# Optimization experiments

Measured on AMD Instinct MI355X. Metric: run time of the kernel, lower is better.

Reference implementation:

```python
import jax, jax.numpy as jnp
import numpy as np

N_NODE = 4095
D_EMB = 32
D_MODEL = 64
NHEADS = 8
ALPHA = 1.0
B = N_NODE + 1  # batch must equal n_node+1 (see einsum 'nm,tmd->tnd')
T = 32


def setup_inputs() -> dict:
    key = jax.random.key(0)
    ks = jax.random.split(key, 16)
    f32 = jnp.float32
    inp = {
        "q": jax.random.normal(ks[0], (B, T, D_MODEL), f32),
        "k": jax.random.normal(ks[1], (B, T, D_MODEL), f32),
        "v": jax.random.normal(ks[2], (B, T, D_MODEL), f32),
        # learned parameters (torch init is randn; scaled for numeric stability)
        "emb": jax.random.normal(ks[3], (N_NODE + 1, D_EMB), f32) * 0.05,
        "We": jax.random.normal(ks[4], (D_EMB, D_MODEL, D_MODEL), f32) * 0.05,
        "be": jax.random.normal(ks[5], (D_EMB, D_MODEL), f32) * 0.05,
        "Wq": jax.random.normal(ks[6], (D_MODEL, D_MODEL), f32) * 0.05,
        "bq": jax.random.normal(ks[7], (D_MODEL,), f32) * 0.05,
        "Wk": jax.random.normal(ks[8], (D_MODEL, D_MODEL), f32) * 0.05,
        "bk": jax.random.normal(ks[9], (D_MODEL,), f32) * 0.05,
        "Wv": jax.random.normal(ks[10], (D_MODEL, D_MODEL), f32) * 0.05,
        "bv": jax.random.normal(ks[11], (D_MODEL,), f32) * 0.05,
        "Wo": jax.random.normal(ks[12], (D_MODEL, D_MODEL), f32) * 0.05,
        "bo": jax.random.normal(ks[13], (D_MODEL,), f32) * 0.05,
    }
    return inp


def _elu(x, alpha):
    return jnp.where(x > 0, x, alpha * (jnp.exp(x) - 1.0))


def _split_heads(x, h):
    # torch.cat(torch.split(x, D//h, dim=-1), dim=0): [B,T,D] -> [h*B,T,D/h]
    b, t, d = x.shape
    return jnp.moveaxis(x.reshape(b, t, h, d // h), 2, 0).reshape(h * b, t, d // h)


def _merge_heads(x, b, h):
    # torch.cat(torch.split(x, B, dim=0), dim=-1): [h*B,T,D/h] -> [B,T,D]
    hb, t, dh = x.shape
    return jnp.moveaxis(x.reshape(h, b, t, dh), 0, 2).reshape(b, t, h * dh)


def reference(q, k, v, emb, We, be, Wq, bq, Wk, bk, Wv, bv, Wo, bo):
    Bq, Tq, D = q.shape
    h = NHEADS
    scale = (D // h) ** 0.5

    # linear projections (torch Linear: x @ W.T + b)
    q = q @ Wq.T + bq
    k = k @ Wk.T + bk
    v = v @ Wv.T + bv

    # adjacency: sum over d_emb of pairwise diff == s_i - s_j (same math, no [N,N,E] tensor)
    s = jnp.sum(emb, axis=-1)  # [N+1]
    sim = s[:, None] - s[None, :]  # [N+1, N+1]
    A = jax.nn.softmax(_elu(sim, ALPHA), axis=-1) + jnp.eye(Bq, dtype=q.dtype)

    # updateQ: adjacency-weighted diffusion + per-node weight matrices
    qt = jnp.transpose(q, (1, 0, 2))  # [T, N, D]
    W = jnp.einsum('ne,eio->nio', emb, We)  # [N, D, D]
    b = emb @ be  # [N, D]
    q_ = jnp.einsum('nm,tmd->tnd', A, qt)  # diffusion
    q_ = jnp.einsum('tnd,ndo->tno', q_, W) + b  # per-node matmul
    q = jnp.transpose(q_, (1, 0, 2))  # [N, T, D]

    # manual multi-head attention via split/cat
    qh = _split_heads(q, h)
    kh = _split_heads(k, h)
    vh = _split_heads(v, h)
    attn = jax.nn.softmax(jnp.einsum('btd,bsd->bts', qh, kh) / scale, axis=-1)
    out = jnp.einsum('bts,bsd->btd', attn, vh)
    out = _merge_heads(out, Bq, h)
    return out @ Wo.T + bo
```

## Files before the change

### kernel.cpp

```cpp
#include <hip/hip_runtime.h>
#include <hip/hip_bf16.h>

constexpr int NN  = 4096;
constexpr int DE  = 32;
constexpr int TD  = 2048;

typedef __attribute__((ext_vector_type(8))) short short8;
typedef __attribute__((ext_vector_type(4))) float f32x4;

#define MFMA16(a, b, c) __builtin_amdgcn_mfma_f32_16x16x32_bf16(a, b, c, 0, 0, 0)

__device__ inline ushort f2b(float x) {
    __hip_bfloat16 h = __float2bfloat16(x);
    union { __hip_bfloat16 h; ushort u; } c; c.h = h;
    return c.u;
}

__device__ inline float b2f(ushort u) {
    union { unsigned u; float f; } c; c.u = ((unsigned)u) << 16;
    return c.f;
}

__device__ inline short8 pack8(float4 a, float4 b) {
    short8 v;
    v[0] = (short)f2b(a.x); v[1] = (short)f2b(a.y); v[2] = (short)f2b(a.z); v[3] = (short)f2b(a.w);
    v[4] = (short)f2b(b.x); v[5] = (short)f2b(b.y); v[6] = (short)f2b(b.z); v[7] = (short)f2b(b.w);
    return v;
}

__device__ inline short8 pack8v(f32x4 a, f32x4 b) {
    short8 v;
    v[0] = (short)f2b(a[0]); v[1] = (short)f2b(a[1]); v[2] = (short)f2b(a[2]); v[3] = (short)f2b(a[3]);
    v[4] = (short)f2b(b[0]); v[5] = (short)f2b(b[1]); v[6] = (short)f2b(b[2]); v[7] = (short)f2b(b[3]);
    return v;
}

__device__ __forceinline__ short8 as_s8(f32x4 v) {
    union { f32x4 f; short8 s; } u; u.f = v; return u.s;
}

template<int OFF>
__device__ __forceinline__ f32x4 gl16(unsigned long long addr) {
    f32x4 d;
    asm volatile("global_load_dwordx4 %0, %1, off offset:%c2"
                 : "=v"(d) : "v"(addr), "n"(OFF) : "memory");
    return d;
}

template<int OFF>
__device__ __forceinline__ float gl4(unsigned long long addr) {
    float d;
    asm volatile("global_load_dword %0, %1, off offset:%c2"
                 : "=v"(d) : "v"(addr), "n"(OFF) : "memory");
    return d;
}

#define WAITV(N) asm volatile("s_waitcnt vmcnt(" #N ")" ::: "memory"); \
                 __builtin_amdgcn_sched_barrier(0)

__global__ __launch_bounds__(256) void k_prep(const float* __restrict__ emb,
                                              const float* __restrict__ We,
                                              const float* __restrict__ be,
                                              const float* __restrict__ Wk,
                                              const float* __restrict__ Wv,
                                              const float* __restrict__ Wo,
                                              float* __restrict__ s_g,
                                              ushort* __restrict__ embbf,
                                              ushort* __restrict__ WeTT,
                                              ushort* __restrict__ Wkbf,
                                              ushort* __restrict__ Wvbf,
                                              ushort* __restrict__ Wobf,
                                              float* __restrict__ bn) {
    int id = blockIdx.x, tid = threadIdx.x;
    if (id < 16) {
        int n = id * 256 + tid;
        const float4* e4 = (const float4*)(emb + n * DE);
        float s = 0.f;
#pragma unroll
        for (int i = 0; i < DE / 4; ++i) { float4 v = e4[i]; s += v.x + v.y + v.z + v.w; }
        s_g[n] = s;
    } else if (id < 144) {
        int g4 = (id - 16) * 256 + tid;
        float4 v = *(const float4*)&emb[(size_t)g4 * 4];
        ushort4 o; o.x = f2b(v.x); o.y = f2b(v.y); o.z = f2b(v.z); o.w = f2b(v.w);
        *(ushort4*)&embbf[(size_t)g4 * 4] = o;
    } else if (id < 176) {
        int e = id - 144;
#pragma unroll
        for (int u = 0; u < 4; ++u) {
            int idx0 = tid * 16 + u * 4;
            float4 v = *(const float4*)&We[(size_t)e * 4096 + idx0];
            float vv[4] = {v.x, v.y, v.z, v.w};
#pragma unroll
            for (int i = 0; i < 4; ++i) {
                int idx = idx0 + i;
                int o = idx & 63, d = idx >> 6;
                WeTT[(size_t)(o * 64 + d) * 32 + e] = f2b(vv[i]);
            }
        }
    } else if (id < 224) {
        int id5 = id - 176;
        int which = id5 >> 4, gid = (id5 & 15) * 256 + tid;
        const float* src = which == 0 ? Wk : (which == 1 ? Wv : Wo);
        ushort* dst = which == 0 ? Wkbf : (which == 1 ? Wvbf : Wobf);
        dst[gid] = f2b(src[gid]);
    } else {
        int gid = (id - 224) * 256 + tid;
        int n = gid >> 6, o = gid & 63;
        float acc = 0.f;
#pragma unroll
        for (int e = 0; e < DE; ++e) acc += emb[n * DE + e] * be[e * 64 + o];
        bn[gid] = acc;
    }
}

__global__ __launch_bounds__(256) void k_pr(const float* __restrict__ X,
                                            const float* __restrict__ W,
                                            const float* __restrict__ bias,
                                            ushort* __restrict__ Y,
                                            const float* __restrict__ s_g,
                                            int* __restrict__ perm) {
    __shared__ float ss[NN];
    int id = blockIdx.x, tid = threadIdx.x;
    if (id < 512) {
        int lane = tid & 63, wid = tid >> 6;
        int r0 = id * 256 + wid * 64;
        int l15 = lane & 15, kb = lane >> 4;
        f32x4 acc[4][4] = {};
#pragma unroll
        for (int kk = 0; kk < 2; ++kk) {
            short8 af[4], bf[4];
#pragma unroll
            for (int f = 0; f < 4; ++f) {
                const float* ap = X + (size_t)(r0 + f * 16 + l15) * 64 + kk * 32 + kb * 8;
                af[f] = pack8(*(const float4*)ap, *(const float4*)(ap + 4));
                const float* bp = W + (size_t)(f * 16 + l15) * 64 + kk * 32 + kb * 8;
                bf[f] = pack8(*(const float4*)bp, *(const float4*)(bp + 4));
            }
#pragma unroll
            for (int i = 0; i < 4; ++i)
#pragma unroll
                for (int j = 0; j < 4; ++j)
                    acc[i][j] = MFMA16(af[i], bf[j], acc[i][j]);
        }
        float bcol[4];
#pragma unroll
        for (int j = 0; j < 4; ++j) bcol[j] = bias[j * 16 + l15];
#pragma unroll
        for (int i = 0; i < 4; ++i)
#pragma unroll
            for (int j = 0; j < 4; ++j)
#pragma unroll
                for (int r = 0; r < 4; ++r)
                    Y[(size_t)(r0 + i * 16 + kb * 4 + r) * 64 + j * 16 + l15] =
                        f2b(acc[i][j][r] + bcol[j]);
    } else {
        for (int i = tid; i < NN; i += 256) ss[i] = s_g[i];
        __syncthreads();
        int g = tid >> 5, l = tid & 31;
        int n = (id - 512) * 8 + g;
        float sn = ss[n];
        int cnt = 0;
        for (int j2 = 0; j2 < 128; ++j2) {
            int m = j2 * 32 + l;
            float sm = ss[m];
            cnt += (sm < sn) || (sm == sn && m < n);
        }
        for (int off = 16; off; off >>= 1) cnt += __shfl_down(cnt, off, 32);
        if (l == 0) perm[cnt] = n;
    }
}

__global__ __launch_bounds__(256) void k_csum(const ushort* __restrict__ qp,
                                              const float* __restrict__ s_g,
                                              const int* __restrict__ perm,
                                              float* __restrict__ Cj,
                                              float* __restrict__ Cb) {
    __shared__ int ns[64];
    __shared__ float bs[64];
    int bx = blockIdx.x, by = blockIdx.y, tid = threadIdx.x;
    if (tid < 64) {
        int n = perm[bx * 64 + tid];
        ns[tid] = n;
        bs[tid] = __expf(-s_g[n]);
    }
    __syncthreads();
    int j = by * 256 + tid;
    float run[8] = {};
    for (int ii = 0; ii < 64; ++ii) {
        float qv = b2f(qp[(size_t)ns[ii] * 2048 + j]);
        float b = bs[ii], t = qv;
#pragma unroll
        for (int k2 = 0; k2 < 8; ++k2) { run[k2] += t; t *= b; }
    }
    float* cp = Cj + ((size_t)bx * 2048 + j) * 8;
    *(float4*)cp       = make_float4(run[0], run[1], run[2], run[3]);
    *(float4*)(cp + 4) = make_float4(run[4], run[5], run[6], run[7]);
    if (by == 0 && tid < 64) {
        float b = bs[tid], bk = 1.f;
#pragma unroll
        for (int k2 = 0; k2 < 8; ++k2) {
            float v = bk;
            for (int off = 32; off; off >>= 1) v += __shfl_down(v, off, 64);
            if (tid == 0) Cb[bx * 8 + k2] = v;
            bk *= b;
        }
    }
}

__global__ __launch_bounds__(256) void k_pre(const float* __restrict__ Cj,
                                             float* __restrict__ PRE,
                                             const float* __restrict__ Cb,
                                             float* __restrict__ CbPre) {
    __shared__ float sCb[512];
    int tid = threadIdx.x;
    if (blockIdx.x < 64) {
        int gid = blockIdx.x * 256 + tid;
        float run = 0.f;
#pragma unroll 8
        for (int c = 0; c < 64; ++c) {
            PRE[(size_t)c * 16384 + gid] = run;
            run += Cj[(size_t)c * 16384 + gid];
        }
        PRE[(size_t)64 * 16384 + gid] = run;
    } else {
        sCb[tid] = Cb[tid];
        sCb[tid + 256] = Cb[tid + 256];
        __syncthreads();
        if (tid < 8) {
            float run = 0.f;
            for (int c = 0; c < 64; ++c) {
                CbPre[c * 8 + tid] = run;
                run += sCb[c * 8 + tid];
            }
            CbPre[512 + tid] = run;
        }
    }
}

__global__ __launch_bounds__(256) void k_combw(const ushort* __restrict__ qp,
                                               const float* __restrict__ s_g,
                                               const int* __restrict__ perm,
                                               const float* __restrict__ PRE,
                                               const float* __restrict__ CbPre,
                                               ushort* __restrict__ qdifb,
                                               const ushort* __restrict__ embbf,
                                               const ushort* __restrict__ WeTT,
                                               ushort* __restrict__ WnT) {
    __shared__ int ns[64];
    __shared__ float sa[64], sb[64];
    int id = blockIdx.x, tid = threadIdx.x;
    if (id < 512) {
        int bx = id & 63, by = id >> 6;
        if (tid < 64) {
            int n = perm[bx * 64 + tid];
            ns[tid] = n;
            float s = s_g[n];
            sa[tid] = __expf(s);
            sb[tid] = __expf(-s);
        }
        __syncthreads();
        int j = by * 256 + tid;
        float T[8], pre[8];
        {
            const float* pp = PRE + (size_t)bx * 16384 + (size_t)j * 8;
            float4 u0 = *(const float4*)pp, u1 = *(const float4*)(pp + 4);
            pre[0] = u0.x; pre[1] = u0.y; pre[2] = u0.z; pre[3] = u0.w;
            pre[4] = u1.x; pre[5] = u1.y; pre[6] = u1.z; pre[7] = u1.w;
            const float* tp = PRE + (size_t)64 * 16384 + (size_t)j * 8;
            float4 t0 = *(const float4*)tp, t1 = *(const float4*)(tp + 4);
            T[0] = t0.x; T[1] = t0.y; T[2] = t0.z; T[3] = t0.w;
            T[4] = t1.x; T[5] = t1.y; T[6] = t1.z; T[7] = t1.w;
        }
        float TB[8], preb[8];
        {
            float4 v0 = *(const float4*)&CbPre[bx * 8], v1 = *(const float4*)&CbPre[bx * 8 + 4];
            preb[0] = v0.x; preb[1] = v0.y; preb[2] = v0.z; preb[3] = v0.w;
            preb[4] = v1.x; preb[5] = v1.y; preb[6] = v1.z; preb[7] = v1.w;
            float4 t0 = *(const float4*)&CbPre[512], t1 = *(const float4*)&CbPre[516];
            TB[0] = t0.x; TB[1] = t0.y; TB[2] = t0.z; TB[3] = t0.w;
            TB[4] = t1.x; TB[5] = t1.y; TB[6] = t1.z; TB[7] = t1.w;
        }
#pragma unroll 2
        for (int ii = 0; ii < 64; ++ii) {
            int n = ns[ii];
            float a = sa[ii], b = sb[ii];
            float g0 = 0.36787944117144233f;
            float g1 = g0 * a;
            float g2 = g1 * a * 0.5f;
            float g3 = g2 * a * (1.f / 3.f);
            float g4 = g3 * a * 0.25f;
            float g5 = g4 * a * 0.2f;
            float g6 = g5 * a * (1.f / 6.f);
            float g7 = g6 * a * (1.f / 7.f);
            float Z = a * preb[1]
                    + g0 * (TB[0] - preb[0]) + g1 * (TB[1] - preb[1])
                    + g2 * (TB[2] - preb[2]) + g3 * (TB[3] - preb[3])
                    + g4 * (TB[4] - preb[4]) + g5 * (TB[5] - preb[5])
                    + g6 * (TB[6] - preb[6]) + g7 * (TB[7] - preb[7]);
            float izv = 1.f / Z;
            float qv = b2f(qp[(size_t)n * 2048 + j]);
            float ss2 = g0 * (T[0] - pre[0]) + g1 * (T[1] - pre[1])
                      + g2 * (T[2] - pre[2]) + g3 * (T[3] - pre[3])
                      + g4 * (T[4] - pre[4]) + g5 * (T[5] - pre[5])
                      + g6 * (T[6] - pre[6]) + g7 * (T[7] - pre[7]);
            float outv = (a * pre[1] + ss2) * izv + qv;
            qdifb[(size_t)n * 2048 + j] = f2b(outv);
            float bk = 1.f;
#pragma unroll
            for (int k2 = 0; k2 < 8; ++k2) { pre[k2] += bk * qv; preb[k2] += bk; bk *= b; }
        }
    } else {
        int w2 = id - 512;
        int lane = tid & 63, wid = tid >> 6;
        int n0  = (w2 & 31) * 128 + (wid >> 1) * 64;
        int od0 = (w2 >> 5) * 128 + (wid & 1) * 64;
        int l15 = lane & 15, kb = lane >> 4;
        short8 af[4], bf[4];
#pragma unroll
        for (int f = 0; f < 4; ++f) {
            af[f] = *(const short8*)(embbf + (size_t)(n0 + f * 16 + l15) * 32 + kb * 8);
            bf[f] = *(const short8*)(WeTT + (size_t)(od0 + f * 16 + l15) * 32 + kb * 8);
        }
        f32x4 acc[4][4] = {};
#pragma unroll
        for (int i = 0; i < 4; ++i)
#pragma unroll
            for (int j = 0; j < 4; ++j)
                acc[i][j] = MFMA16(af[i], bf[j], acc[i][j]);
#pragma unroll
        for (int i = 0; i < 4; ++i)
#pragma unroll
            for (int j = 0; j < 4; ++j)
#pragma unroll
                for (int r = 0; r < 4; ++r)
                    WnT[(size_t)(n0 + i * 16 + kb * 4 + r) * 4096 + od0 + j * 16 + l15] =
                        f2b(acc[i][j][r]);
    }
}

__global__ __launch_bounds__(128, 2) void k_fused(const float* __restrict__ kin,
                                                  const float* __restrict__ vin,
                                                  const ushort* __restrict__ qdifb,
                                                  const ushort* __restrict__ WnT,
                                                  const float* __restrict__ bn,
                                                  const ushort* __restrict__ Wkbf,
                                                  const float* __restrict__ bk,
                                                  const ushort* __restrict__ Wvbf,
                                                  const float* __restrict__ bv,
                                                  const ushort* __restrict__ Wobf,
                                                  const float* __restrict__ bo,
                                                  float* __restrict__ out) {
    __shared__ ushort Kb[2][2176];
    __shared__ ushort Qb[2][2176];
    __shared__ ushort Vb[2][2560];
    __shared__ ushort Pb[2][1280];
    __shared__ ushort attb[2][2304];
    int tid = threadIdx.x, lane = tid & 63, w = tid >> 6;
    int b = blockIdx.x * 2 + w;
    int l15 = lane & 15, g = lane >> 4;
    int hh_w = l15 >> 3, d1_w = l15 & 7;
    const float SCALE = 0.35355339059327373f;
    short8 zfrag = {};

    unsigned long long bkA = (unsigned long long)(bk + 32 + l15);
    unsigned long long bnA = (unsigned long long)(bn + (size_t)b * 64 + 32 + l15);
    unsigned long long bvA = (unsigned long long)(bv + 32 + l15);
    unsigned long long boA = (unsigned long long)(bo + 32 + l15);
    unsigned long long wkA = (unsigned long long)((const char*)Wkbf + l15 * 128 + g * 16 + 3072);
    unsigned long long kaA = (unsigned long long)(kin + (size_t)b * TD + (8 + l15) * 64 + g * 8);
    unsigned long long wvA = (unsigned long long)((const char*)Wvbf + l15 * 128 + g * 16 + 3072);
    unsigned long long vaA = (unsigned long long)(vin + (size_t)b * TD + (8 + l15) * 64 + g * 8);
    unsigned long long qaA = (unsigned long long)(qdifb + (size_t)b * TD + (8 + l15) * 64 + g * 8);
    unsigned long long waA = (unsigned long long)(WnT + (size_t)b * 4096 + (24 + l15) * 64 + g * 8);
    unsigned long long woA = (unsigned long long)((const char*)Wobf + l15 * 128 + g * 16 + 3072);

    float bkc[4], bnc[4], bvc[4], boc[4];
    bkc[0] = gl4<-128>(bkA); bkc[1] = gl4<-64>(bkA); bkc[2] = gl4<0>(bkA); bkc[3] = gl4<64>(bkA);
    bnc[0] = gl4<-128>(bnA); bnc[1] = gl4<-64>(bnA); bnc[2] = gl4<0>(bnA); bnc[3] = gl4<64>(bnA);
    bvc[0] = gl4<-128>(bvA); bvc[1] = gl4<-64>(bvA); bvc[2] = gl4<0>(bvA); bvc[3] = gl4<64>(bvA);
    boc[0] = gl4<-128>(boA); boc[1] = gl4<-64>(boA); boc[2] = gl4<0>(boA); boc[3] = gl4<64>(boA);
    f32x4 wk00 = gl16<-3072>(wkA), wk01 = gl16<-3008>(wkA);
    f32x4 wk10 = gl16<-1024>(wkA), wk11 = gl16< -960>(wkA);
    f32x4 wk20 = gl16< 1024>(wkA), wk21 = gl16< 1088>(wkA);
    f32x4 wk30 = gl16< 3072>(wkA), wk31 = gl16< 3136>(wkA);
    f32x4 k00a = gl16<-2048>(kaA), k00b = gl16<-2032>(kaA);
    f32x4 k01a = gl16<-1920>(kaA), k01b = gl16<-1904>(kaA);
    f32x4 k10a = gl16< 2048>(kaA), k10b = gl16< 2064>(kaA);
    f32x4 k11a = gl16< 2176>(kaA), k11b = gl16< 2192>(kaA);
    f32x4 wv00 = gl16<-3072>(wvA), wv01 = gl16<-3008>(wvA);
    f32x4 wv10 = gl16<-1024>(wvA), wv11 = gl16< -960>(wvA);
    f32x4 wv20 = gl16< 1024>(wvA), wv21 = gl16< 1088>(wvA);
    f32x4 wv30 = gl16< 3072>(wvA), wv31 = gl16< 3136>(wvA);
    f32x4 v00a = gl16<-2048>(vaA), v00b = gl16<-2032>(vaA);
    f32x4 v01a = gl16<-1920>(vaA), v01b = gl16<-1904>(vaA);
    f32x4 v10a = gl16< 2048>(vaA), v10b = gl16< 2064>(vaA);
    f32x4 v11a = gl16< 2176>(vaA), v11b = gl16< 2192>(vaA);

    WAITV(16);
    {
        short8 kaf[2][2], wkf[4][2];
        kaf[0][0] = pack8v(k00a, k00b); kaf[1][0] = pack8v(k01a, k01b);
        kaf[0][1] = pack8v(k10a, k10b); kaf[1][1] = pack8v(k11a, k11b);
        wkf[0][0] = as_s8(wk00); wkf[0][1] = as_s8(wk01);
        wkf[1][0] = as_s8(wk10); wkf[1][1] = as_s8(wk11);
        wkf[2][0] = as_s8(wk20); wkf[2][1] = as_s8(wk21);
        wkf[3][0] = as_s8(wk30); wkf[3][1] = as_s8(wk31);
#pragma unroll
        for (int j = 0; j < 4; ++j) {
            f32x4 ak[2] = {};
#pragma unroll
            for (int kk = 0; kk < 2; ++kk)
#pragma unroll
                for (int ti = 0; ti < 2; ++ti)
                    ak[ti] = MFMA16(kaf[kk][ti], wkf[j][kk], ak[ti]);
#pragma unroll
            for (int ti = 0; ti < 2; ++ti)
#pragma unroll
                for (int r = 0; r < 4; ++r) {
                    int s = ti * 16 + g * 4 + r;
                    Kb[w][(j * 2 + hh_w) * 272 + s * 8 + d1_w] = f2b(ak[ti][r] + bkc[j]);
                }
        }
    }

    f32x4 q00 = gl16<-1024>(qaA), q01 = gl16<-960>(qaA);
    f32x4 q10 = gl16< 1024>(qaA), q11 = gl16<1088>(qaA);
    f32x4 w00 = gl16<-3072>(waA), w01 = gl16<-3008>(waA);
    f32x4 w10 = gl16<-1024>(waA), w11 = gl16< -960>(waA);
    f32x4 w20 = gl16< 1024>(waA), w21 = gl16< 1088>(waA);
    f32x4 w30 = gl16< 3072>(waA), w31 = gl16< 3136>(waA);

    WAITV(12);
    {
        short8 vaf[2][2], wvf[4][2];
        vaf[0][0] = pack8v(v00a, v00b); vaf[1][0] = pack8v(v01a, v01b);
        vaf[0][1] = pack8v(v10a, v10b); vaf[1][1] = pack8v(v11a, v11b);
        wvf[0][0] = as_s8(wv00); wvf[0][1] = as_s8(wv01);
        wvf[1][0] = as_s8(wv10); wvf[1][1] = as_s8(wv11);
        wvf[2][0] = as_s8(wv20); wvf[2][1] = as_s8(wv21);
        wvf[3][0] = as_s8(wv30); wvf[3][1] = as_s8(wv31);
#pragma unroll
        for (int j = 0; j < 4; ++j) {
            f32x4 av[2] = {};
#pragma unroll
            for (int kk = 0; kk < 2; ++kk)
#pragma unroll
                for (int ti = 0; ti < 2; ++ti)
                    av[ti] = MFMA16(vaf[kk][ti], wvf[j][kk], av[ti]);
#pragma unroll
            for (int ti = 0; ti < 2; ++ti)
#pragma unroll
                for (int r = 0; r < 4; r += 2) {
                    int s = ti * 16 + g * 4 + r;
                    ushort2 p; p.x = f2b(av[ti][r] + bvc[j]); p.y = f2b(av[ti][r + 1] + bvc[j]);
                    *(ushort2*)&Vb[w][(j * 2 + hh_w) * 320 + d1_w * 40 + s] = p;
                }
        }
    }

    f32x4 wo00 = gl16<-3072>(woA), wo01 = gl16<-3008>(woA);
    f32x4 wo10 = gl16<-1024>(woA), wo11 = gl16< -960>(woA);
    f32x4 wo20 = gl16< 1024>(woA), wo21 = gl16< 1088>(woA);
    f32x4 wo30 = gl16< 3072>(woA), wo31 = gl16< 3136>(woA);

    WAITV(8);
    {
        short8 qaf[2][2], bqf[4][2];
        qaf[0][0] = as_s8(q00); qaf[1][0] = as_s8(q01);
        qaf[0][1] = as_s8(q10); qaf[1][1] = as_s8(q11);
        bqf[0][0] = as_s8(w00); bqf[0][1] = as_s8(w01);
        bqf[1][0] = as_s8(w10); bqf[1][1] = as_s8(w11);
        bqf[2][0] = as_s8(w20); bqf[2][1] = as_s8(w21);
        bqf[3][0] = as_s8(w30); bqf[3][1] = as_s8(w31);
#pragma unroll
        for (int j = 0; j < 4; ++j) {
            f32x4 aq[2] = {};
#pragma unroll
            for (int kk = 0; kk < 2; ++kk)
#pragma unroll
                for (int ti = 0; ti < 2; ++ti)
                    aq[ti] = MFMA16(qaf[kk][ti], bqf[j][kk], aq[ti]);
#pragma unroll
            for (int ti = 0; ti < 2; ++ti)
#pragma unroll
                for (int r = 0; r < 4; ++r) {
                    int s = ti * 16 + g * 4 + r;
                    Qb[w][(j * 2 + hh_w) * 272 + s * 8 + d1_w] = f2b(aq[ti][r] + bnc[j]);
                }
        }
    }

#pragma unroll
    for (int h = 0; h < 8; ++h) {
        short8 kf[2], qf[2];
#pragma unroll
        for (int si = 0; si < 2; ++si)
            kf[si] = (lane < 16) ? *(const short8*)&Kb[w][h * 272 + (si * 16 + l15) * 8] : zfrag;
#pragma unroll
        for (int ti = 0; ti < 2; ++ti)
            qf[ti] = (lane < 16) ? *(const short8*)&Qb[w][h * 272 + (ti * 16 + l15) * 8] : zfrag;
        f32x4 sc[2][2];
#pragma unroll
        for (int si = 0; si < 2; ++si)
#pragma unroll
            for (int ti = 0; ti < 2; ++ti)
                sc[si][ti] = MFMA16(kf[si], qf[ti], f32x4{});
#pragma unroll
        for (int ti = 0; ti < 2; ++ti) {
            float e0[4], e1[4], sm = 0.f;
#pragma unroll
            for (int r = 0; r < 4; ++r) {
                e0[r] = __expf(sc[0][ti][r] * SCALE);
                e1[r] = __expf(sc[1][ti][r] * SCALE);
                sm += e0[r] + e1[r];
            }
            sm += __shfl_xor(sm, 16);
            sm += __shfl_xor(sm, 32);
            float inv = 1.f / sm;
            int t = ti * 16 + l15;
            unsigned p00 = (unsigned)f2b(e0[0] * inv) | ((unsigned)f2b(e0[1] * inv) << 16);
            unsigned p01 = (unsigned)f2b(e0[2] * inv) | ((unsigned)f2b(e0[3] * inv) << 16);
            unsigned p10 = (unsigned)f2b(e1[0] * inv) | ((unsigned)f2b(e1[1] * inv) << 16);
            unsigned p11 = (unsigned)f2b(e1[2] * inv) | ((unsigned)f2b(e1[3] * inv) << 16);
            *(unsigned*)&Pb[w][t * 40 + g * 4]          = p00;
            *(unsigned*)&Pb[w][t * 40 + g * 4 + 2]      = p01;
            *(unsigned*)&Pb[w][t * 40 + 16 + g * 4]     = p10;
            *(unsigned*)&Pb[w][t * 40 + 16 + g * 4 + 2] = p11;
        }
        short8 vf = *(const short8*)&Vb[w][h * 320 + (l15 & 7) * 40 + g * 8];
#pragma unroll
        for (int ti = 0; ti < 2; ++ti) {
            short8 af = *(const short8*)&Pb[w][(ti * 16 + l15) * 40 + g * 8];
            f32x4 pv = MFMA16(af, vf, f32x4{});
            if (l15 < 8) {
#pragma unroll
                for (int r = 0; r < 4; ++r)
                    attb[w][(ti * 16 + g * 4 + r) * 72 + h * 8 + l15] = f2b(pv[r]);
            }
        }
    }

    WAITV(0);
    {
        short8 wof[4][2];
        wof[0][0] = as_s8(wo00); wof[0][1] = as_s8(wo01);
        wof[1][0] = as_s8(wo10); wof[1][1] = as_s8(wo11);
        wof[2][0] = as_s8(wo20); wof[2][1] = as_s8(wo21);
        wof[3][0] = as_s8(wo30); wof[3][1] = as_s8(wo31);
        short8 aof[2][2];
#pragma unroll
        for (int kk = 0; kk < 2; ++kk)
#pragma unroll
            for (int ti = 0; ti < 2; ++ti)
                aof[kk][ti] = *(const short8*)&attb[w][(ti * 16 + l15) * 72 + kk * 32 + g * 8];
        f32x4 co[2][4] = {};
#pragma unroll
        for (int kk = 0; kk < 2; ++kk)
#pragma unroll
            for (int j = 0; j < 4; ++j)
#pragma unroll
                for (int ti = 0; ti < 2; ++ti)
                    co[ti][j] = MFMA16(aof[kk][ti], wof[j][kk], co[ti][j]);
#pragma unroll
        for (int ti = 0; ti < 2; ++ti)
#pragma unroll
            for (int j = 0; j < 4; ++j)
#pragma unroll
                for (int r = 0; r < 4; ++r)
                    out[(size_t)b * TD + (ti * 16 + g * 4 + r) * 64 + j * 16 + l15] =
                        co[ti][j][r] + boc[j];
    }
}

extern "C" void kernel_launch(void* const* d_in, const int* in_sizes, int n_in,
                              void* d_out, int out_size, void* d_ws, size_t ws_size,
                              hipStream_t stream) {
    const float* q   = (const float*)d_in[0];
    const float* k   = (const float*)d_in[1];
    const float* v   = (const float*)d_in[2];
    const float* emb = (const float*)d_in[3];
    const float* We  = (const float*)d_in[4];
    const float* be  = (const float*)d_in[5];
    const float* Wq  = (const float*)d_in[6];
    const float* bq  = (const float*)d_in[7];
    const float* Wk  = (const float*)d_in[8];
    const float* bk  = (const float*)d_in[9];
    const float* Wv  = (const float*)d_in[10];
    const float* bv  = (const float*)d_in[11];
    const float* Wo  = (const float*)d_in[12];
    const float* bo  = (const float*)d_in[13];

    float* ws = (float*)d_ws;
    ushort* qp    = (ushort*)ws;
    ushort* WnT   = (ushort*)(ws + 4194304);
    ushort* qdifb = (ushort*)(ws + 12582912);
    float*  Cj    = ws + 16777216;
    float*  bn    = ws + 17825792;
    float*  s_g   = ws + 18087936;
    int*    perm  = (int*)(ws + 18092032);
    float*  Cb    = ws + 18096128;
    ushort* embbf = (ushort*)(ws + 18096640);
    ushort* WeTT  = (ushort*)(ws + 18162176);
    ushort* Wkbf  = (ushort*)(ws + 18227712);
    ushort* Wvbf  = (ushort*)(ws + 18229760);
    ushort* Wobf  = (ushort*)(ws + 18231808);
    float*  PRE   = ws + 18233856;
    float*  CbPre = ws + 19298816;
    float*  outp  = (float*)d_out;

    k_prep <<<1248, 256, 0, stream>>>(emb, We, be, Wk, Wv, Wo,
                                      s_g, embbf, WeTT, Wkbf, Wvbf, Wobf, bn);
    k_pr   <<<1024, 256, 0, stream>>>(q, Wq, bq, qp, s_g, perm);
    k_csum <<<dim3(64, 8), 256, 0, stream>>>(qp, s_g, perm, Cj, Cb);
    k_pre  <<<65, 256, 0, stream>>>(Cj, PRE, Cb, CbPre);
    k_combw<<<1536, 256, 0, stream>>>(qp, s_g, perm, PRE, CbPre, qdifb,
                                      embbf, WeTT, WnT);
    k_fused<<<2048, 128, 0, stream>>>(k, v, qdifb, WnT, bn,
                                      Wkbf, bk, Wvbf, bv, Wobf, bo, outp);
}
```

Baseline: 114.8 us.

## Split each batch item across two waves in fused attention kernel

The fused attention kernel previously gave each wave a whole batch item, with two items per block. Now each block handles one item. Wave 0 projects K and wave 1 projects V, and each wave computes half the Q output columns, half the heads and half the output projection columns, with two barriers through shared LDS buffers. This halves per-wave serial work and register pressure and doubles the grid to 4096 blocks, at the cost of block-level synchronisation and more blocks to schedule.

New measurement: 109.9 us. -4.2%, faster.

```diff
diff --git a/kernel.cpp b/kernel.cpp
--- a/kernel.cpp
+++ b/kernel.cpp
@@ -351,155 +351,125 @@
                                                   const ushort* __restrict__ Wobf,
                                                   const float* __restrict__ bo,
                                                   float* __restrict__ out) {
-    __shared__ ushort Kb[2][2176];
-    __shared__ ushort Qb[2][2176];
-    __shared__ ushort Vb[2][2560];
+    __shared__ ushort Kb[2176];
+    __shared__ ushort Qb[2176];
+    __shared__ ushort Vb[2560];
     __shared__ ushort Pb[2][1280];
-    __shared__ ushort attb[2][2304];
+    __shared__ ushort attb[2304];
     int tid = threadIdx.x, lane = tid & 63, w = tid >> 6;
-    int b = blockIdx.x * 2 + w;
+    int b = blockIdx.x;
     int l15 = lane & 15, g = lane >> 4;
     int hh_w = l15 >> 3, d1_w = l15 & 7;
     const float SCALE = 0.35355339059327373f;
     short8 zfrag = {};
 
-    unsigned long long bkA = (unsigned long long)(bk + 32 + l15);
-    unsigned long long bnA = (unsigned long long)(bn + (size_t)b * 64 + 32 + l15);
-    unsigned long long bvA = (unsigned long long)(bv + 32 + l15);
-    unsigned long long boA = (unsigned long long)(bo + 32 + l15);
-    unsigned long long wkA = (unsigned long long)((const char*)Wkbf + l15 * 128 + g * 16 + 3072);
-    unsigned long long kaA = (unsigned long long)(kin + (size_t)b * TD + (8 + l15) * 64 + g * 8);
-    unsigned long long wvA = (unsigned long long)((const char*)Wvbf + l15 * 128 + g * 16 + 3072);
-    unsigned long long vaA = (unsigned long long)(vin + (size_t)b * TD + (8 + l15) * 64 + g * 8);
+    const float*  xin = w ? vin : kin;
+    const ushort* Wx  = w ? Wvbf : Wkbf;
+    const float*  bx_ = w ? bv : bk;
+
+    unsigned long long bxA = (unsigned long long)(bx_ + l15);
+    unsigned long long bnA = (unsigned long long)(bn + (size_t)b * 64 + w * 32 + l15);
+    unsigned long long boA = (unsigned long long)(bo + w * 32 + l15);
+    unsigned long long wxA = (unsigned long long)((const char*)Wx + l15 * 128 + g * 16 + 3072);
+    unsigned long long xaA = (unsigned long long)(xin + (size_t)b * TD + (8 + l15) * 64 + g * 8);
     unsigned long long qaA = (unsigned long long)(qdifb + (size_t)b * TD + (8 + l15) * 64 + g * 8);
-    unsigned long long waA = (unsigned long long)(WnT + (size_t)b * 4096 + (24 + l15) * 64 + g * 8);
-    unsigned long long woA = (unsigned long long)((const char*)Wobf + l15 * 128 + g * 16 + 3072);
-
-    float bkc[4], bnc[4], bvc[4], boc[4];
-    bkc[0] = gl4<-128>(bkA); bkc[1] = gl4<-64>(bkA); bkc[2] = gl4<0>(bkA); bkc[3] = gl4<64>(bkA);
-    bnc[0] = gl4<-128>(bnA); bnc[1] = gl4<-64>(bnA); bnc[2] = gl4<0>(bnA); bnc[3] = gl4<64>(bnA);
-    bvc[0] = gl4<-128>(bvA); bvc[1] = gl4<-64>(bvA); bvc[2] = gl4<0>(bvA); bvc[3] = gl4<64>(bvA);
-    boc[0] = gl4<-128>(boA); boc[1] = gl4<-64>(boA); boc[2] = gl4<0>(boA); boc[3] = gl4<64>(boA);
-    f32x4 wk00 = gl16<-3072>(wkA), wk01 = gl16<-3008>(wkA);
-    f32x4 wk10 = gl16<-1024>(wkA), wk11 = gl16< -960>(wkA);
-    f32x4 wk20 = gl16< 1024>(wkA), wk21 = gl16< 1088>(wkA);
-    f32x4 wk30 = gl16< 3072>(wkA), wk31 = gl16< 3136>(wkA);
-    f32x4 k00a = gl16<-2048>(kaA), k00b = gl16<-2032>(kaA);
-    f32x4 k01a = gl16<-1920>(kaA), k01b = gl16<-1904>(kaA);
-    f32x4 k10a = gl16< 2048>(kaA), k10b = gl16< 2064>(kaA);
-    f32x4 k11a = gl16< 2176>(kaA), k11b = gl16< 2192>(kaA);
-    f32x4 wv00 = gl16<-3072>(wvA), wv01 = gl16<-3008>(wvA);
-    f32x4 wv10 = gl16<-1024>(wvA), wv11 = gl16< -960>(wvA);
-    f32x4 wv20 = gl16< 1024>(wvA), wv21 = gl16< 1088>(wvA);
-    f32x4 wv30 = gl16< 3072>(wvA), wv31 = gl16< 3136>(wvA);
-    f32x4 v00a = gl16<-2048>(vaA), v00b = gl16<-2032>(vaA);
-    f32x4 v01a = gl16<-1920>(vaA), v01b = gl16<-1904>(vaA);
-    f32x4 v10a = gl16< 2048>(vaA), v10b = gl16< 2064>(vaA);
-    f32x4 v11a = gl16< 2176>(vaA), v11b = gl16< 2192>(vaA);
-
-    WAITV(16);
+    unsigned long long wnA = (unsigned long long)((const char*)(WnT + (size_t)b * 4096) + w * 4096 + l15 * 128 + g * 16 + 1024);
+    unsigned long long woA = (unsigned long long)((const char*)Wobf + w * 4096 + l15 * 128 + g * 16 + 1024);
+
+    float bxc[4], bnc[2], boc[2];
+    bxc[0] = gl4<0>(bxA); bxc[1] = gl4<64>(bxA); bxc[2] = gl4<128>(bxA); bxc[3] = gl4<192>(bxA);
+    bnc[0] = gl4<0>(bnA); bnc[1] = gl4<64>(bnA);
+    boc[0] = gl4<0>(boA); boc[1] = gl4<64>(boA);
+    f32x4 wx00 = gl16<-3072>(wxA), wx01 = gl16<-3008>(wxA);
+    f32x4 wx10 = gl16<-1024>(wxA), wx11 = gl16< -960>(wxA);
+    f32x4 wx20 = gl16< 1024>(wxA), wx21 = gl16< 1088>(wxA);
+    f32x4 wx30 = gl16< 3072>(wxA), wx31 = gl16< 3136>(wxA);
+    f32x4 x00a = gl16<-2048>(xaA), x00b = gl16<-2032>(xaA);
+    f32x4 x01a = gl16<-1920>(xaA), x01b = gl16<-1904>(xaA);
+    f32x4 x10a = gl16< 2048>(xaA), x10b = gl16< 2064>(xaA);
+    f32x4 x11a = gl16< 2176>(xaA), x11b = gl16< 2192>(xaA);
+    f32x4 q00 = gl16<-1024>(qaA), q01 = gl16<-960>(qaA);
+    f32x4 q10 = gl16< 1024>(qaA), q11 = gl16<1088>(qaA);
+    f32x4 wn00 = gl16<-1024>(wnA), wn01 = gl16<-960>(wnA);
+    f32x4 wn10 = gl16< 1024>(wnA), wn11 = gl16<1088>(wnA);
+    f32x4 wo00 = gl16<-1024>(woA), wo01 = gl16<-960>(woA);
+    f32x4 wo10 = gl16< 1024>(woA), wo11 = gl16<1088>(woA);
+
+    WAITV(12);
     {
-        short8 kaf[2][2], wkf[4][2];
-        kaf[0][0] = pack8v(k00a, k00b); kaf[1][0] = pack8v(k01a, k01b);
-        kaf[0][1] = pack8v(k10a, k10b); kaf[1][1] = pack8v(k11a, k11b);
-        wkf[0][0] = as_s8(wk00); wkf[0][1] = as_s8(wk01);
-        wkf[1][0] = as_s8(wk10); wkf[1][1] = as_s8(wk11);
-        wkf[2][0] = as_s8(wk20); wkf[2][1] = as_s8(wk21);
-        wkf[3][0] = as_s8(wk30); wkf[3][1] = as_s8(wk31);
+        short8 xaf[2][2], wxf[4][2];
+        xaf[0][0] = pack8v(x00a, x00b); xaf[1][0] = pack8v(x01a, x01b);
+        xaf[0][1] = pack8v(x10a, x10b); xaf[1][1] = pack8v(x11a, x11b);
+        wxf[0][0] = as_s8(wx00); wxf[0][1] = as_s8(wx01);
+        wxf[1][0] = as_s8(wx10); wxf[1][1] = as_s8(wx11);
+        wxf[2][0] = as_s8(wx20); wxf[2][1] = as_s8(wx21);
+        wxf[3][0] = as_s8(wx30); wxf[3][1] = as_s8(wx31);
 #pragma unroll
         for (int j = 0; j < 4; ++j) {
-            f32x4 ak[2] = {};
+            f32x4 ax[2] = {};
 #pragma unroll
             for (int kk = 0; kk < 2; ++kk)
 #pragma unroll
                 for (int ti = 0; ti < 2; ++ti)
-                    ak[ti] = MFMA16(kaf[kk][ti], wkf[j][kk], ak[ti]);
+                    ax[ti] = MFMA16(xaf[kk][ti], wxf[j][kk], ax[ti]);
+            if (w == 0) {
+#pragma unroll
+                for (int ti = 0; ti < 2; ++ti)
+#pragma unroll
+                    for (int r = 0; r < 4; ++r) {
+                        int s = ti * 16 + g * 4 + r;
+                        Kb[(j * 2 + hh_w) * 272 + s * 8 + d1_w] = f2b(ax[ti][r] + bxc[j]);
+                    }
+            } else {
+#pragma unroll
+                for (int ti = 0; ti < 2; ++ti)
+#pragma unroll
+                    for (int r = 0; r < 4; r += 2) {
+                        int s = ti * 16 + g * 4 + r;
+                        ushort2 p; p.x = f2b(ax[ti][r] + bxc[j]); p.y = f2b(ax[ti][r + 1] + bxc[j]);
+                        *(ushort2*)&Vb[(j * 2 + hh_w) * 320 + d1_w * 40 + s] = p;
+                    }
+            }
+        }
+    }
+
+    WAITV(4);
+    {
+        short8 qaf[2][2], wnf[2][2];
+        qaf[0][0] = as_s8(q00); qaf[1][0] = as_s8(q01);
+        qaf[0][1] = as_s8(q10); qaf[1][1] = as_s8(q11);
+        wnf[0][0] = as_s8(wn00); wnf[0][1] = as_s8(wn01);
+        wnf[1][0] = as_s8(wn10); wnf[1][1] = as_s8(wn11);
+#pragma unroll
+        for (int jj = 0; jj < 2; ++jj) {
+            int j = 2 * w + jj;
+            f32x4 aq[2] = {};
+#pragma unroll
+            for (int kk = 0; kk < 2; ++kk)
+#pragma unroll
+                for (int ti = 0; ti < 2; ++ti)
+                    aq[ti] = MFMA16(qaf[kk][ti], wnf[jj][kk], aq[ti]);
 #pragma unroll
             for (int ti = 0; ti < 2; ++ti)
 #pragma unroll
                 for (int r = 0; r < 4; ++r) {
                     int s = ti * 16 + g * 4 + r;
-                    Kb[w][(j * 2 + hh_w) * 272 + s * 8 + d1_w] = f2b(ak[ti][r] + bkc[j]);
+                    Qb[(j * 2 + hh_w) * 272 + s * 8 + d1_w] = f2b(aq[ti][r] + bnc[jj]);
                 }
         }
     }
-
-    f32x4 q00 = gl16<-1024>(qaA), q01 = gl16<-960>(qaA);
-    f32x4 q10 = gl16< 1024>(qaA), q11 = gl16<1088>(qaA);
-    f32x4 w00 = gl16<-3072>(waA), w01 = gl16<-3008>(waA);
-    f32x4 w10 = gl16<-1024>(waA), w11 = gl16< -960>(waA);
-    f32x4 w20 = gl16< 1024>(waA), w21 = gl16< 1088>(waA);
-    f32x4 w30 = gl16< 3072>(waA), w31 = gl16< 3136>(waA);
-
-    WAITV(12);
-    {
-        short8 vaf[2][2], wvf[4][2];
-        vaf[0][0] = pack8v(v00a, v00b); vaf[1][0] = pack8v(v01a, v01b);
-        vaf[0][1] = pack8v(v10a, v10b); vaf[1][1] = pack8v(v11a, v11b);
-        wvf[0][0] = as_s8(wv00); wvf[0][1] = as_s8(wv01);
-        wvf[1][0] = as_s8(wv10); wvf[1][1] = as_s8(wv11);
-        wvf[2][0] = as_s8(wv20); wvf[2][1] = as_s8(wv21);
-        wvf[3][0] = as_s8(wv30); wvf[3][1] = as_s8(wv31);
-#pragma unroll
-        for (int j = 0; j < 4; ++j) {
-            f32x4 av[2] = {};
-#pragma unroll
-            for (int kk = 0; kk < 2; ++kk)
-#pragma unroll
-                for (int ti = 0; ti < 2; ++ti)
-                    av[ti] = MFMA16(vaf[kk][ti], wvf[j][kk], av[ti]);
-#pragma unroll
-            for (int ti = 0; ti < 2; ++ti)
-#pragma unroll
-                for (int r = 0; r < 4; r += 2) {
-                    int s = ti * 16 + g * 4 + r;
-                    ushort2 p; p.x = f2b(av[ti][r] + bvc[j]); p.y = f2b(av[ti][r + 1] + bvc[j]);
-                    *(ushort2*)&Vb[w][(j * 2 + hh_w) * 320 + d1_w * 40 + s] = p;
-                }
-        }
-    }
-
-    f32x4 wo00 = gl16<-3072>(woA), wo01 = gl16<-3008>(woA);
-    f32x4 wo10 = gl16<-1024>(woA), wo11 = gl16< -960>(woA);
-    f32x4 wo20 = gl16< 1024>(woA), wo21 = gl16< 1088>(woA);
-    f32x4 wo30 = gl16< 3072>(woA), wo31 = gl16< 3136>(woA);
-
-    WAITV(8);
-    {
-        short8 qaf[2][2], bqf[4][2];
-        qaf[0][0] = as_s8(q00); qaf[1][0] = as_s8(q01);
-        qaf[0][1] = as_s8(q10); qaf[1][1] = as_s8(q11);
-        bqf[0][0] = as_s8(w00); bqf[0][1] = as_s8(w01);
-        bqf[1][0] = as_s8(w10); bqf[1][1] = as_s8(w11);
-        bqf[2][0] = as_s8(w20); bqf[2][1] = as_s8(w21);
-        bqf[3][0] = as_s8(w30); bqf[3][1] = as_s8(w31);
-#pragma unroll
-        for (int j = 0; j < 4; ++j) {
-            f32x4 aq[2] = {};
-#pragma unroll
-            for (int kk = 0; kk < 2; ++kk)
-#pragma unroll
-                for (int ti = 0; ti < 2; ++ti)
-                    aq[ti] = MFMA16(qaf[kk][ti], bqf[j][kk], aq[ti]);
-#pragma unroll
-            for (int ti = 0; ti < 2; ++ti)
-#pragma unroll
-                for (int r = 0; r < 4; ++r) {
-                    int s = ti * 16 + g * 4 + r;
-                    Qb[w][(j * 2 + hh_w) * 272 + s * 8 + d1_w] = f2b(aq[ti][r] + bnc[j]);
-                }
-        }
-    }
-
-#pragma unroll
-    for (int h = 0; h < 8; ++h) {
+    __syncthreads();
+
+#pragma unroll
+    for (int hh = 0; hh < 4; ++hh) {
+        int h = 4 * w + hh;
         short8 kf[2], qf[2];
 #pragma unroll
         for (int si = 0; si < 2; ++si)
-            kf[si] = (lane < 16) ? *(const short8*)&Kb[w][h * 272 + (si * 16 + l15) * 8] : zfrag;
+            kf[si] = (lane < 16) ? *(const short8*)&Kb[h * 272 + (si * 16 + l15) * 8] : zfrag;
 #pragma unroll
         for (int ti = 0; ti < 2; ++ti)
-            qf[ti] = (lane < 16) ? *(const short8*)&Qb[w][h * 272 + (ti * 16 + l15) * 8] : zfrag;
+            qf[ti] = (lane < 16) ? *(const short8*)&Qb[h * 272 + (ti * 16 + l15) * 8] : zfrag;
         f32x4 sc[2][2];
 #pragma unroll
         for (int si = 0; si < 2; ++si)
@@ -528,7 +498,7 @@
             *(unsigned*)&Pb[w][t * 40 + 16 + g * 4]     = p10;
             *(unsigned*)&Pb[w][t * 40 + 16 + g * 4 + 2] = p11;
         }
-        short8 vf = *(const short8*)&Vb[w][h * 320 + (l15 & 7) * 40 + g * 8];
+        short8 vf = *(const short8*)&Vb[h * 320 + (l15 & 7) * 40 + g * 8];
 #pragma unroll
         for (int ti = 0; ti < 2; ++ti) {
             short8 af = *(const short8*)&Pb[w][(ti * 16 + l15) * 40 + g * 8];
@@ -536,40 +506,39 @@
             if (l15 < 8) {
 #pragma unroll
                 for (int r = 0; r < 4; ++r)
-                    attb[w][(ti * 16 + g * 4 + r) * 72 + h * 8 + l15] = f2b(pv[r]);
+                    attb[(ti * 16 + g * 4 + r) * 72 + h * 8 + l15] = f2b(pv[r]);
             }
         }
     }
+    __syncthreads();
 
     WAITV(0);
     {
-        short8 wof[4][2];
+        short8 wof[2][2];
         wof[0][0] = as_s8(wo00); wof[0][1] = as_s8(wo01);
         wof[1][0] = as_s8(wo10); wof[1][1] = as_s8(wo11);
-        wof[2][0] = as_s8(wo20); wof[2][1] = as_s8(wo21);
-        wof[3][0] = as_s8(wo30); wof[3][1] = as_s8(wo31);
         short8 aof[2][2];
 #pragma unroll
         for (int kk = 0; kk < 2; ++kk)
 #pragma unroll
             for (int ti = 0; ti < 2; ++ti)
-                aof[kk][ti] = *(const short8*)&attb[w][(ti * 16 + l15) * 72 + kk * 32 + g * 8];
-        f32x4 co[2][4] = {};
-#pragma unroll
-        for (int kk = 0; kk < 2; ++kk)
-#pragma unroll
-            for (int j = 0; j < 4; ++j)
+                aof[kk][ti] = *(const short8*)&attb[(ti * 16 + l15) * 72 + kk * 32 + g * 8];
+#pragma unroll
+        for (int jj = 0; jj < 2; ++jj) {
+            int j = 2 * w + jj;
+            f32x4 co[2] = {};
+#pragma unroll
+            for (int kk = 0; kk < 2; ++kk)
 #pragma unroll
                 for (int ti = 0; ti < 2; ++ti)
-                    co[ti][j] = MFMA16(aof[kk][ti], wof[j][kk], co[ti][j]);
-#pragma unroll
-        for (int ti = 0; ti < 2; ++ti)
-#pragma unroll
-            for (int j = 0; j < 4; ++j)
+                    co[ti] = MFMA16(aof[kk][ti], wof[jj][kk], co[ti]);
+#pragma unroll
+            for (int ti = 0; ti < 2; ++ti)
 #pragma unroll
                 for (int r = 0; r < 4; ++r)
                     out[(size_t)b * TD + (ti * 16 + g * 4 + r) * 64 + j * 16 + l15] =
-                        co[ti][j][r] + boc[j];
+                        co[ti][r] + boc[jj];
+        }
     }
 }
 
@@ -616,6 +585,6 @@
     k_pre  <<<65, 256, 0, stream>>>(Cj, PRE, Cb, CbPre);
     k_combw<<<1536, 256, 0, stream>>>(qp, s_g, perm, PRE, CbPre, qdifb,
                                       embbf, WeTT, WnT);
-    k_fused<<<2048, 128, 0, stream>>>(k, v, qdifb, WnT, bn,
+    k_fused<<<4096, 128, 0, stream>>>(k, v, qdifb, WnT, bn,
                                       Wkbf, bk, Wvbf, bv, Wobf, bo, outp);
 }
```
